# Performance work log

Hardware: AMD Instinct MI355X
Metric: run time of the kernel (lower is better)

## Reference

```python
import jax, jax.numpy as jnp
import numpy as np
import math

RES = 1024
HEADS = 16
HEAD_RES = RES // HEADS
B, S = 2, 2048


def setup_inputs() -> dict:
    key = jax.random.key(0)
    kx, kq, kk, kv = jax.random.split(key, 4)
    scale = 1.0 / math.sqrt(RES)
    return {
        "x": jax.random.normal(kx, (B, S, RES), dtype=jnp.float32),
        "Wq": jax.random.normal(kq, (RES, RES), dtype=jnp.float32) * scale,
        "Wk": jax.random.normal(kk, (RES, RES), dtype=jnp.float32) * scale,
        "Wv": jax.random.normal(kv, (RES, RES), dtype=jnp.float32) * scale,
    }


def reference(x, Wq, Wk, Wv):
    batch, seq, _ = x.shape
    # projections (torch Linear without bias: x @ W.T; here W stored as [in, out])
    def split_heads(t):
        return t.reshape(batch, seq, HEADS, HEAD_RES).transpose(0, 2, 1, 3)  # [B,H,S,D]
    q = split_heads(x @ Wq)
    k = split_heads(x @ Wk)
    v = split_heads(x @ Wv)
    scores = jnp.einsum("bhsd,bhtd->bhst", q, k) / math.sqrt(HEAD_RES)
    attn = jax.nn.softmax(scores, axis=-1)
    out = jnp.einsum("bhst,bhtd->bhsd", attn, v)  # [B,H,S,D]
    return out.transpose(0, 2, 1, 3).reshape(batch, seq, RES)
```

## Files before the change

kernel.cpp:

```cpp
#include <hip/hip_runtime.h>

typedef _Float16 f16;
typedef _Float16 half4 __attribute__((ext_vector_type(4)));
typedef _Float16 half8 __attribute__((ext_vector_type(8)));
typedef float f32x4 __attribute__((ext_vector_type(4)));

#define RES 1024
#define NH 16
#define HD 64
#define BATCH 2
#define SEQ 2048
#define M_ROWS (BATCH * SEQ)

__device__ __forceinline__ void gload_lds16(const void* g, void* l) {
  __builtin_amdgcn_global_load_lds(
      (const __attribute__((address_space(1))) unsigned int*)g,
      (__attribute__((address_space(3))) unsigned int*)l, 16, 0, 0);
}

__global__ __launch_bounds__(1024) void prep_kernel(const float* __restrict__ x,
                                                    const float* __restrict__ Wq,
                                                    const float* __restrict__ Wk,
                                                    const float* __restrict__ Wv,
                                                    f16* __restrict__ xh,
                                                    f16* __restrict__ Wt) {
  __shared__ float tile[32][33];
  int bx = blockIdx.x;
  int tid = threadIdx.x;
  if (bx < 3072) {
    int wz = bx >> 10;
    int rem = bx & 1023;
    int bxx = rem & 31, byy = rem >> 5;
    const float* W = wz == 0 ? Wq : (wz == 1 ? Wk : Wv);
    f16* Wo = Wt + (size_t)wz * RES * RES;
    int txx = tid & 31, tyy = tid >> 5;
    int n = bxx * 32 + txx;
    int k = byy * 32 + tyy;
    tile[tyy][txx] = W[(size_t)k * RES + n];
    __syncthreads();
    int ko = byy * 32 + txx;
    int no = bxx * 32 + tyy;
    Wo[(size_t)no * RES + ko] = (f16)tile[txx][tyy];
  } else {
    int idx = (bx - 3072) * 1024 + tid;
    const float4* xv = (const float4*)x;
    float4 a = xv[idx * 2];
    float4 b = xv[idx * 2 + 1];
    half8 h;
    h[0] = (f16)a.x; h[1] = (f16)a.y; h[2] = (f16)a.z; h[3] = (f16)a.w;
    h[4] = (f16)b.x; h[5] = (f16)b.y; h[6] = (f16)b.z; h[7] = (f16)b.w;
    ((half8*)xh)[idx] = h;
  }
}

__global__ __launch_bounds__(256) void proj_gemm_kernel(const f16* __restrict__ xh,
                                                        const f16* __restrict__ Wt,
                                                        f16* __restrict__ Qh,
                                                        f16* __restrict__ Kh,
                                                        f16* __restrict__ Vt) {
  int proj = blockIdx.z;
  const f16* Bt = Wt + (size_t)proj * RES * RES;
  int m0 = blockIdx.x * 128;
  int n0 = blockIdx.y * 128;
  __shared__ alignas(16) f16 Als[128 * 32];
  __shared__ alignas(16) f16 Bls[128 * 32];
  int t = threadIdx.x, lane = t & 63, w = t >> 6;
  int l15 = lane & 15, quad = lane >> 4;
  int wm = w >> 1, wn = w & 1;

  f32x4 zero = {0.f, 0.f, 0.f, 0.f};
  f32x4 acc[4][4];
#pragma unroll
  for (int i = 0; i < 4; i++)
#pragma unroll
    for (int j = 0; j < 4; j++) acc[i][j] = zero;

  bool tr = (proj != 2);

  for (int k0 = 0; k0 < RES; k0 += 32) {
#pragma unroll
    for (int i = 0; i < 2; i++) {
      int wl = i * 256 + w * 64;
      int linear = wl + lane;
      int row = linear >> 2;
      int kk = (linear & 3) * 8;
      gload_lds16(xh + (size_t)(m0 + row) * RES + k0 + kk, &Als[wl * 8]);
      gload_lds16(Bt + (size_t)(n0 + row) * RES + k0 + kk, &Bls[wl * 8]);
    }
    __syncthreads();
    half8 af[4], bf[4];
#pragma unroll
    for (int mt = 0; mt < 4; mt++)
      af[mt] = *(const half8*)&Als[(wm * 64 + mt * 16 + l15) * 32 + quad * 8];
#pragma unroll
    for (int nt = 0; nt < 4; nt++)
      bf[nt] = *(const half8*)&Bls[(wn * 64 + nt * 16 + l15) * 32 + quad * 8];
    if (tr) {
#pragma unroll
      for (int i = 0; i < 4; i++)
#pragma unroll
        for (int j = 0; j < 4; j++)
          acc[i][j] = __builtin_amdgcn_mfma_f32_16x16x32_f16(bf[i], af[j], acc[i][j], 0, 0, 0);
    } else {
#pragma unroll
      for (int i = 0; i < 4; i++)
#pragma unroll
        for (int j = 0; j < 4; j++)
          acc[i][j] = __builtin_amdgcn_mfma_f32_16x16x32_f16(af[i], bf[j], acc[i][j], 0, 0, 0);
    }
    __syncthreads();
  }

  if (tr) {
    f16* dst = proj ? Kh : Qh;
#pragma unroll
    for (int i = 0; i < 4; i++) {
#pragma unroll
      for (int j = 0; j < 4; j++) {
        int n = n0 + wn * 64 + i * 16 + quad * 4;
        int m = m0 + wm * 64 + j * 16 + l15;
        int b = m >> 11, s = m & (SEQ - 1);
        int h = n >> 6, d = n & (HD - 1);
        size_t bh = (size_t)b * NH + h;
        half4 v;
#pragma unroll
        for (int r = 0; r < 4; r++) v[r] = (f16)acc[i][j][r];
        *(half4*)&dst[(bh * SEQ + s) * HD + d] = v;
      }
    }
  } else {
#pragma unroll
    for (int i = 0; i < 4; i++) {
#pragma unroll
      for (int j = 0; j < 4; j++) {
        int m = m0 + wm * 64 + i * 16 + quad * 4;
        int n = n0 + wn * 64 + j * 16 + l15;
        int b = m >> 11, s = m & (SEQ - 1);
        int h = n >> 6, d = n & (HD - 1);
        size_t bh = (size_t)b * NH + h;
        half4 v;
#pragma unroll
        for (int r = 0; r < 4; r++) v[r] = (f16)acc[i][j][r];
        *(half4*)&Vt[(bh * HD + d) * SEQ + s] = v;
      }
    }
  }
}

__global__ __launch_bounds__(128, 3) void flash_kernel(const f16* __restrict__ Qh,
                                                       const f16* __restrict__ Kh,
                                                       const f16* __restrict__ Vt,
                                                       float* __restrict__ out) {
  constexpr int PSTR = 72;
  int L = blockIdx.x;
  int xcd = L & 7, slot = L >> 3;
  int bh = ((slot >> 5) << 3) | xcd;
  int qt = slot & 31;
  int b = bh >> 4, h = bh & 15;
  int tid = threadIdx.x;
  int lane = tid & 63, w = tid >> 6;
  int l15 = lane & 15, quad = lane >> 4;
  int qrow0 = qt * 64 + w * 32;

  __shared__ alignas(16) f16 Kls[64 * 64];
  __shared__ alignas(16) f16 Vls[64 * 64];
  __shared__ alignas(16) f16 p_lds[2][32 * PSTR];

  const f16* kbase = Kh + (size_t)bh * SEQ * HD;
  const f16* vbase = Vt + (size_t)bh * HD * SEQ;

  int srow = tid >> 3;
  int schunk = tid & 7;

  const f16 SCALE = (f16)(0.125f * 1.44269504f);
  const f16* qptr = Qh + ((size_t)bh * SEQ + qrow0 + l15) * HD + quad * 8;
  half8 qf[2][2];
  qf[0][0] = *(const half8*)qptr;
  qf[0][1] = *(const half8*)(qptr + 32);
  qf[1][0] = *(const half8*)(qptr + 16 * HD);
  qf[1][1] = *(const half8*)(qptr + 16 * HD + 32);
#pragma unroll
  for (int q2 = 0; q2 < 2; q2++)
#pragma unroll
    for (int ks = 0; ks < 2; ks++)
#pragma unroll
      for (int j = 0; j < 8; j++) qf[q2][ks][j] *= SCALE;

  f32x4 zero = {0.f, 0.f, 0.f, 0.f};
  float l_acc[2] = {0.f, 0.f};
  f32x4 o[2][4];
#pragma unroll
  for (int q2 = 0; q2 < 2; q2++)
#pragma unroll
    for (int nt = 0; nt < 4; nt++) o[q2][nt] = zero;

  int swz0 = (quad ^ (l15 & 7)) * 8;
  int swz1 = ((quad + 4) ^ (l15 & 7)) * 8;

  for (int kv0 = 0; kv0 < SEQ; kv0 += 64) {
#pragma unroll
    for (int rd = 0; rd < 4; rd++) {
      int row = rd * 16 + srow;
      int pc = schunk ^ (row & 7);
      gload_lds16(kbase + ((size_t)(kv0 + row) << 6) + pc * 8,
                  &Kls[rd * 1024 + w * 512]);
      gload_lds16(vbase + ((size_t)row * SEQ) + kv0 + pc * 8,
                  &Vls[rd * 1024 + w * 512]);
    }
    __syncthreads();

    half8 kf0[4], kf1[4];
#pragma unroll
    for (int tt = 0; tt < 4; tt++) {
      int row = tt * 16 + l15;
      kf0[tt] = *(const half8*)&Kls[row * 64 + swz0];
      kf1[tt] = *(const half8*)&Kls[row * 64 + swz1];
    }
#pragma unroll
    for (int q2 = 0; q2 < 2; q2++) {
      f32x4 sc[4];
#pragma unroll
      for (int tt = 0; tt < 4; tt++) {
        sc[tt] = __builtin_amdgcn_mfma_f32_16x16x32_f16(kf0[tt], qf[q2][0], zero, 0, 0, 0);
        sc[tt] = __builtin_amdgcn_mfma_f32_16x16x32_f16(kf1[tt], qf[q2][1], sc[tt], 0, 0, 0);
      }
      float ps = 0.f;
#pragma unroll
      for (int tt = 0; tt < 4; tt++)
#pragma unroll
        for (int r = 0; r < 4; r++) {
          sc[tt][r] = __builtin_amdgcn_exp2f(sc[tt][r]);
          ps += sc[tt][r];
        }
      ps += __shfl_xor(ps, 16);
      ps += __shfl_xor(ps, 32);
      l_acc[q2] += ps;
#pragma unroll
      for (int tt = 0; tt < 4; tt++) {
        half4 pk;
        pk[0] = (f16)sc[tt][0]; pk[1] = (f16)sc[tt][1];
        pk[2] = (f16)sc[tt][2]; pk[3] = (f16)sc[tt][3];
        *(half4*)&p_lds[w][(q2 * 16 + l15) * PSTR + tt * 16 + quad * 4] = pk;
      }
    }
    half8 vf0[4], vf1[4];
#pragma unroll
    for (int nt = 0; nt < 4; nt++) {
      int row = nt * 16 + l15;
      vf0[nt] = *(const half8*)&Vls[row * 64 + swz0];
      vf1[nt] = *(const half8*)&Vls[row * 64 + swz1];
    }
#pragma unroll
    for (int q2 = 0; q2 < 2; q2++) {
#pragma unroll
      for (int ks = 0; ks < 2; ks++) {
        half8 pf = *(const half8*)&p_lds[w][(q2 * 16 + l15) * PSTR + ks * 32 + quad * 8];
#pragma unroll
        for (int nt = 0; nt < 4; nt++)
          o[q2][nt] = __builtin_amdgcn_mfma_f32_16x16x32_f16(pf, ks ? vf1[nt] : vf0[nt], o[q2][nt], 0, 0, 0);
      }
    }
    __syncthreads();
  }

#pragma unroll
  for (int q2 = 0; q2 < 2; q2++) {
    float linv[4];
#pragma unroll
    for (int r = 0; r < 4; r++) linv[r] = 1.0f / __shfl(l_acc[q2], quad * 4 + r);
#pragma unroll
    for (int nt = 0; nt < 4; nt++) {
#pragma unroll
      for (int r = 0; r < 4; r++) {
        int s = qrow0 + q2 * 16 + quad * 4 + r;
        out[((size_t)b * SEQ + s) * RES + h * HD + nt * 16 + l15] = o[q2][nt][r] * linv[r];
      }
    }
  }
}

extern "C" void kernel_launch(void* const* d_in, const int* in_sizes, int n_in,
                              void* d_out, int out_size, void* d_ws, size_t ws_size,
                              hipStream_t stream) {
  (void)in_sizes; (void)n_in; (void)out_size; (void)ws_size;
  const float* x  = (const float*)d_in[0];
  const float* Wq = (const float*)d_in[1];
  const float* Wk = (const float*)d_in[2];
  const float* Wv = (const float*)d_in[3];
  float* out = (float*)d_out;

  f16* xh = (f16*)d_ws;
  f16* Wt = xh + (size_t)M_ROWS * RES;
  f16* Qh = Wt + (size_t)3 * RES * RES;
  f16* Kh = Qh + (size_t)BATCH * NH * SEQ * HD;
  f16* Vt = Kh + (size_t)BATCH * NH * SEQ * HD;

  prep_kernel<<<3584, 1024, 0, stream>>>(x, Wq, Wk, Wv, xh, Wt);
  proj_gemm_kernel<<<dim3(M_ROWS / 128, RES / 128, 3), 256, 0, stream>>>(xh, Wt, Qh, Kh, Vt);
  flash_kernel<<<1024, 128, 0, stream>>>(Qh, Kh, Vt, out);
}
```

Measured before the change: 185.9 us.

## Halve flash attention query tile to 32 rows and double the grid

Each flash block now covers 32 query rows (16 per wave) instead of 64, and the grid doubles to 2048 blocks. The block-to-(bh, query tile) mapping is updated to match, and the P staging buffer shrinks. The goal is more blocks and waves per CU, giving better occupancy and latency hiding across the 256 CUs. The cost is that every K/V tile is loaded from global memory into LDS twice as often per query row, and MFMA reuse of the K and V fragments per LDS load is halved.

Result: slower. 200.3 us (+7.8%).

```diff
diff --git a/kernel.cpp b/kernel.cpp
--- a/kernel.cpp
+++ b/kernel.cpp
@@ -154,17 +154,17 @@
   constexpr int PSTR = 72;
   int L = blockIdx.x;
   int xcd = L & 7, slot = L >> 3;
-  int bh = ((slot >> 5) << 3) | xcd;
-  int qt = slot & 31;
+  int bh = ((slot >> 6) << 3) | xcd;
+  int qt = slot & 63;
   int b = bh >> 4, h = bh & 15;
   int tid = threadIdx.x;
   int lane = tid & 63, w = tid >> 6;
   int l15 = lane & 15, quad = lane >> 4;
-  int qrow0 = qt * 64 + w * 32;
+  int qrow0 = qt * 32 + w * 16;
 
   __shared__ alignas(16) f16 Kls[64 * 64];
   __shared__ alignas(16) f16 Vls[64 * 64];
-  __shared__ alignas(16) f16 p_lds[2][32 * PSTR];
+  __shared__ alignas(16) f16 p_lds[2][16 * PSTR];
 
   const f16* kbase = Kh + (size_t)bh * SEQ * HD;
   const f16* vbase = Vt + (size_t)bh * HD * SEQ;
@@ -174,25 +174,16 @@
 
   const f16 SCALE = (f16)(0.125f * 1.44269504f);
   const f16* qptr = Qh + ((size_t)bh * SEQ + qrow0 + l15) * HD + quad * 8;
-  half8 qf[2][2];
-  qf[0][0] = *(const half8*)qptr;
-  qf[0][1] = *(const half8*)(qptr + 32);
-  qf[1][0] = *(const half8*)(qptr + 16 * HD);
-  qf[1][1] = *(const half8*)(qptr + 16 * HD + 32);
-#pragma unroll
-  for (int q2 = 0; q2 < 2; q2++)
-#pragma unroll
-    for (int ks = 0; ks < 2; ks++)
-#pragma unroll
-      for (int j = 0; j < 8; j++) qf[q2][ks][j] *= SCALE;
+  half8 qf0 = *(const half8*)qptr;
+  half8 qf1 = *(const half8*)(qptr + 32);
+#pragma unroll
+  for (int j = 0; j < 8; j++) { qf0[j] *= SCALE; qf1[j] *= SCALE; }
 
   f32x4 zero = {0.f, 0.f, 0.f, 0.f};
-  float l_acc[2] = {0.f, 0.f};
-  f32x4 o[2][4];
-#pragma unroll
-  for (int q2 = 0; q2 < 2; q2++)
-#pragma unroll
-    for (int nt = 0; nt < 4; nt++) o[q2][nt] = zero;
+  float l_acc = 0.f;
+  f32x4 o[4];
+#pragma unroll
+  for (int i = 0; i < 4; i++) o[i] = zero;
 
   int swz0 = (quad ^ (l15 & 7)) * 8;
   int swz1 = ((quad + 4) ^ (l15 & 7)) * 8;
@@ -216,32 +207,11 @@
       kf0[tt] = *(const half8*)&Kls[row * 64 + swz0];
       kf1[tt] = *(const half8*)&Kls[row * 64 + swz1];
     }
-#pragma unroll
-    for (int q2 = 0; q2 < 2; q2++) {
-      f32x4 sc[4];
-#pragma unroll
-      for (int tt = 0; tt < 4; tt++) {
-        sc[tt] = __builtin_amdgcn_mfma_f32_16x16x32_f16(kf0[tt], qf[q2][0], zero, 0, 0, 0);
-        sc[tt] = __builtin_amdgcn_mfma_f32_16x16x32_f16(kf1[tt], qf[q2][1], sc[tt], 0, 0, 0);
-      }
-      float ps = 0.f;
-#pragma unroll
-      for (int tt = 0; tt < 4; tt++)
-#pragma unroll
-        for (int r = 0; r < 4; r++) {
-          sc[tt][r] = __builtin_amdgcn_exp2f(sc[tt][r]);
-          ps += sc[tt][r];
-        }
-      ps += __shfl_xor(ps, 16);
-      ps += __shfl_xor(ps, 32);
-      l_acc[q2] += ps;
-#pragma unroll
-      for (int tt = 0; tt < 4; tt++) {
-        half4 pk;
-        pk[0] = (f16)sc[tt][0]; pk[1] = (f16)sc[tt][1];
-        pk[2] = (f16)sc[tt][2]; pk[3] = (f16)sc[tt][3];
-        *(half4*)&p_lds[w][(q2 * 16 + l15) * PSTR + tt * 16 + quad * 4] = pk;
-      }
+    f32x4 sc[4];
+#pragma unroll
+    for (int tt = 0; tt < 4; tt++) {
+      sc[tt] = __builtin_amdgcn_mfma_f32_16x16x32_f16(kf0[tt], qf0, zero, 0, 0, 0);
+      sc[tt] = __builtin_amdgcn_mfma_f32_16x16x32_f16(kf1[tt], qf1, sc[tt], 0, 0, 0);
     }
     half8 vf0[4], vf1[4];
 #pragma unroll
@@ -250,31 +220,43 @@
       vf0[nt] = *(const half8*)&Vls[row * 64 + swz0];
       vf1[nt] = *(const half8*)&Vls[row * 64 + swz1];
     }
-#pragma unroll
-    for (int q2 = 0; q2 < 2; q2++) {
-#pragma unroll
-      for (int ks = 0; ks < 2; ks++) {
-        half8 pf = *(const half8*)&p_lds[w][(q2 * 16 + l15) * PSTR + ks * 32 + quad * 8];
-#pragma unroll
-        for (int nt = 0; nt < 4; nt++)
-          o[q2][nt] = __builtin_amdgcn_mfma_f32_16x16x32_f16(pf, ks ? vf1[nt] : vf0[nt], o[q2][nt], 0, 0, 0);
+    float ps = 0.f;
+#pragma unroll
+    for (int tt = 0; tt < 4; tt++)
+#pragma unroll
+      for (int r = 0; r < 4; r++) {
+        sc[tt][r] = __builtin_amdgcn_exp2f(sc[tt][r]);
+        ps += sc[tt][r];
       }
-    }
-    __syncthreads();
-  }
-
-#pragma unroll
-  for (int q2 = 0; q2 < 2; q2++) {
-    float linv[4];
-#pragma unroll
-    for (int r = 0; r < 4; r++) linv[r] = 1.0f / __shfl(l_acc[q2], quad * 4 + r);
-#pragma unroll
-    for (int nt = 0; nt < 4; nt++) {
-#pragma unroll
-      for (int r = 0; r < 4; r++) {
-        int s = qrow0 + q2 * 16 + quad * 4 + r;
-        out[((size_t)b * SEQ + s) * RES + h * HD + nt * 16 + l15] = o[q2][nt][r] * linv[r];
-      }
+    ps += __shfl_xor(ps, 16);
+    ps += __shfl_xor(ps, 32);
+    l_acc += ps;
+#pragma unroll
+    for (int tt = 0; tt < 4; tt++) {
+      half4 pk;
+      pk[0] = (f16)sc[tt][0]; pk[1] = (f16)sc[tt][1];
+      pk[2] = (f16)sc[tt][2]; pk[3] = (f16)sc[tt][3];
+      *(half4*)&p_lds[w][l15 * PSTR + tt * 16 + quad * 4] = pk;
+    }
+#pragma unroll
+    for (int ks = 0; ks < 2; ks++) {
+      half8 pf = *(const half8*)&p_lds[w][l15 * PSTR + ks * 32 + quad * 8];
+#pragma unroll
+      for (int nt = 0; nt < 4; nt++)
+        o[nt] = __builtin_amdgcn_mfma_f32_16x16x32_f16(pf, ks ? vf1[nt] : vf0[nt], o[nt], 0, 0, 0);
+    }
+    __syncthreads();
+  }
+
+  float linv[4];
+#pragma unroll
+  for (int r = 0; r < 4; r++) linv[r] = 1.0f / __shfl(l_acc, quad * 4 + r);
+#pragma unroll
+  for (int nt = 0; nt < 4; nt++) {
+#pragma unroll
+    for (int r = 0; r < 4; r++) {
+      int s = qrow0 + quad * 4 + r;
+      out[((size_t)b * SEQ + s) * RES + h * HD + nt * 16 + l15] = o[nt][r] * linv[r];
     }
   }
 }
@@ -297,5 +279,5 @@
 
   prep_kernel<<<3584, 1024, 0, stream>>>(x, Wq, Wk, Wv, xh, Wt);
   proj_gemm_kernel<<<dim3(M_ROWS / 128, RES / 128, 3), 256, 0, stream>>>(xh, Wt, Qh, Kh, Vt);
-  flash_kernel<<<1024, 128, 0, stream>>>(Qh, Kh, Vt, out);
-}
+  flash_kernel<<<2048, 128, 0, stream>>>(Qh, Kh, Vt, out);
+}
```
